# Optimization experiments

Hardware: AMD Instinct MI355X
Metric: run time of the kernel (lower is better)

## Reference

```python
import jax, jax.numpy as jnp
import numpy as np

B, N, M, C = 8, 8192, 2048, 256
EPS = 1e-8


def setup_inputs() -> dict:
    key = jax.random.key(0)
    k1, k2, k3 = jax.random.split(key, 3)
    unknown = jax.random.uniform(k1, (B, N, 3), dtype=jnp.float32)
    known = jax.random.uniform(k2, (B, M, 3), dtype=jnp.float32)
    known_feats = jax.random.normal(k3, (B, C, M), dtype=jnp.float32)
    return {"unknown": unknown, "known": known, "known_feats": known_feats}


def reference(unknown, known, known_feats):
    # three_nn: brute-force squared distances (B, n, m); pointnet2's CUDA
    # three_nn returns SQUARED distances, matching 1/(d2 + eps) weighting.
    diff = unknown[:, :, None, :] - known[:, None, :, :]  # (B, n, m, 3)
    d2 = jnp.sum(diff * diff, axis=-1)                    # (B, n, m)
    neg_d2, idx = jax.lax.top_k(-d2, 3)                   # 3 smallest distances
    dist = -neg_d2                                        # (B, n, 3)
    dist_recip = 1.0 / (dist + EPS)
    weight = dist_recip / jnp.sum(dist_recip, axis=2, keepdims=True)  # (B, n, 3)
    # three_interpolate: gather the 3 neighbor features and weighted-sum.
    feats_t = jnp.swapaxes(known_feats, 1, 2)             # (B, m, C)
    gathered = jax.vmap(lambda f, i: f[i])(feats_t, idx)  # (B, n, 3, C)
    new_features = jnp.einsum("bnkc,bnk->bcn", gathered, weight)  # (B, C, n)
    return new_features
```

## Files before the change

kernel.cpp:

```cpp
#include <hip/hip_runtime.h>


#define BB 8
#define NN 8192
#define MM 2048
#define CC 256
#define EPSV 1e-8f
#define NTH 512
#define NCH 8
#define CHUNK (MM/NCH)
#define PTS 64
#define MARGIN 1e-4f
#define TC 4

#define INS(dd, mi, D0,I0,D1,I1,D2,I2) \
    if ((dd) < D2) { \
        if ((dd) < D1) { D2 = D1; I2 = I1; \
            if ((dd) < D0) { D1 = D0; I1 = I0; D0 = (dd); I0 = (mi); } \
            else           { D1 = (dd); I1 = (mi); } \
        } else { D2 = (dd); I2 = (mi); } }

#define RF(KX,KY,KZ,KQ) \
    __fmaf_rn((KZ), az, __fmaf_rn((KY), ay, __fmaf_rn((KX), ax, (KQ))))

#define S1(KX,KY,KZ,KQ) { \
    const float rr = RF(KX,KY,KZ,KQ); \
    R2 = __builtin_amdgcn_fmed3f(R1, R2, rr); \
    R1 = __builtin_amdgcn_fmed3f(R0, R1, rr); \
    R0 = fminf(R0, rr); }

#define CAP(RR,KX,KY,KZ,MI) \
    if ((RR) <= Tm) { \
        const float dx = ux-(KX), dy = uy-(KY), dz = uz-(KZ); \
        const float d = __fadd_rn(__fadd_rn(__fmul_rn(dx,dx),__fmul_rn(dy,dy)),__fmul_rn(dz,dz)); \
        INS(d, MI, D0,J0,D1,J1,D2,J2) }

typedef unsigned short u16;

__global__ __launch_bounds__(NTH) void nn_scan_kernel(
    const float* __restrict__ unknown,
    const float* __restrict__ known,
    float4* __restrict__ wgt4,
    int4*  __restrict__ idx4)
{
    __shared__ float kxs[MM], kys[MM], kzs[MM], kqs[MM];
    __shared__ float pd[NCH][PTS][3];
    __shared__ u16   si[NCH][PTS][3];
    __shared__ float Tarr[PTS];

    const int tilesPerBatch = NN / PTS;
    const int b    = blockIdx.x / tilesPerBatch;
    const int tile = blockIdx.x % tilesPerBatch;
    const int t    = threadIdx.x;
    const int lane = t & 63;
    const int g    = t >> 6;

    const float* kb = known + (size_t)b * MM * 3;
    for (int idx = t; idx < MM * 3; idx += NTH) {
        const float v  = kb[idx];
        const int   a  = idx % 3;
        const int   mi = idx / 3;
        float* dst = (a == 0) ? kxs : ((a == 1) ? kys : kzs);
        dst[mi] = v;
    }
    __syncthreads();
    for (int m = t; m < MM; m += NTH) {
        const float x = kxs[m], y = kys[m], z = kzs[m];
        kqs[m] = __fmaf_rn(z, z, __fmaf_rn(y, y, x * x));
    }

    const float* u = unknown + ((size_t)b * NN + (size_t)tile * PTS + lane) * 3;
    const float ux = u[0], uy = u[1], uz = u[2];
    const float ax = -2.0f * ux, ay = -2.0f * uy, az = -2.0f * uz;
    __syncthreads();

    float R0 = 1e30f, R1 = 1e30f, R2 = 1e30f;
    const int mbeg = g * CHUNK;
    #pragma unroll 4
    for (int m = mbeg; m < mbeg + CHUNK; m += 4) {
        const float4 x4 = *reinterpret_cast<const float4*>(&kxs[m]);
        const float4 y4 = *reinterpret_cast<const float4*>(&kys[m]);
        const float4 z4 = *reinterpret_cast<const float4*>(&kzs[m]);
        const float4 q4 = *reinterpret_cast<const float4*>(&kqs[m]);
        S1(x4.x, y4.x, z4.x, q4.x)
        S1(x4.y, y4.y, z4.y, q4.y)
        S1(x4.z, y4.z, z4.z, q4.z)
        S1(x4.w, y4.w, z4.w, q4.w)
    }
    pd[g][lane][0] = R0; pd[g][lane][1] = R1; pd[g][lane][2] = R2;
    __syncthreads();

    if (t < PTS) {
        float e0 = 1e30f, e1 = 1e30f, e2 = 1e30f;
        #pragma unroll
        for (int q = 0; q < NCH; ++q) {
            #pragma unroll
            for (int r = 0; r < 3; ++r) {
                const float d = pd[q][t][r];
                e2 = __builtin_amdgcn_fmed3f(e1, e2, d);
                e1 = __builtin_amdgcn_fmed3f(e0, e1, d);
                e0 = fminf(e0, d);
            }
        }
        Tarr[t] = e2 + MARGIN;
    }
    __syncthreads();

    float D0 = 1e30f, D1 = 1e30f, D2 = 1e30f;
    int   J0 = 0,     J1 = 0,     J2 = 0;
    const float Tm = Tarr[lane];

    #pragma unroll 2
    for (int m = mbeg; m < mbeg + CHUNK; m += 4) {
        const float4 x4 = *reinterpret_cast<const float4*>(&kxs[m]);
        const float4 y4 = *reinterpret_cast<const float4*>(&kys[m]);
        const float4 z4 = *reinterpret_cast<const float4*>(&kzs[m]);
        const float4 q4 = *reinterpret_cast<const float4*>(&kqs[m]);
        const float rr0 = RF(x4.x, y4.x, z4.x, q4.x);
        const float rr1 = RF(x4.y, y4.y, z4.y, q4.y);
        const float rr2 = RF(x4.z, y4.z, z4.z, q4.z);
        const float rr3 = RF(x4.w, y4.w, z4.w, q4.w);
        if (fminf(fminf(rr0, rr1), fminf(rr2, rr3)) <= Tm) {
            CAP(rr0, x4.x, y4.x, z4.x, m)
            CAP(rr1, x4.y, y4.y, z4.y, m+1)
            CAP(rr2, x4.z, y4.z, z4.z, m+2)
            CAP(rr3, x4.w, y4.w, z4.w, m+3)
        }
    }

    pd[g][lane][0] = D0; pd[g][lane][1] = D1; pd[g][lane][2] = D2;
    si[g][lane][0] = (u16)J0; si[g][lane][1] = (u16)J1; si[g][lane][2] = (u16)J2;
    __syncthreads();

    if (t < PTS) {
        float e0 = 1e30f, e1 = 1e30f, e2 = 1e30f;
        int   j0 = 0,     j1 = 0,     j2 = 0;
        #pragma unroll
        for (int q = 0; q < NCH; ++q) {
            #pragma unroll
            for (int r = 0; r < 3; ++r) {
                const float d  = pd[q][t][r];
                const int   ii = (int)si[q][t][r];
                INS(d, ii, e0,j0,e1,j1,e2,j2)
            }
        }
        const float r0 = 1.0f / (e0 + EPSV);
        const float r1 = 1.0f / (e1 + EPSV);
        const float r2 = 1.0f / (e2 + EPSV);
        const float rs = r0 + r1 + r2;
        const int gp = b * NN + tile * PTS + t;
        wgt4[gp] = make_float4(r0 / rs, r1 / rs, r2 / rs, 0.0f);
        idx4[gp] = make_int4(j0, j1, j2, 0);
    }
}

__global__ __launch_bounds__(NTH) void interp_kernel(
    const float* __restrict__ feats,
    const float4* __restrict__ wgt4,
    const int4*  __restrict__ idx4,
    float* __restrict__ out)
{
    __shared__ float fbuf[TC * MM];

    const int tilesPerB = CC / TC;
    const int b  = blockIdx.x / tilesPerB;
    const int c0 = (blockIdx.x % tilesPerB) * TC;
    const int t  = threadIdx.x;

    const float4* src = reinterpret_cast<const float4*>(
        feats + ((size_t)b * CC + c0) * MM);
    #pragma unroll
    for (int i = t; i < TC * MM / 4; i += NTH)
        reinterpret_cast<float4*>(fbuf)[i] = src[i];
    __syncthreads();

    #pragma unroll 2
    for (int it = 0; it < NN / NTH; ++it) {
        const int n = it * NTH + t;
        const float4 w = wgt4[b * NN + n];
        const int4   j = idx4[b * NN + n];
        float* ob = out + ((size_t)b * CC + c0) * NN + n;
        #pragma unroll
        for (int cl = 0; cl < TC; ++cl) {
            const float* fr = fbuf + cl * MM;
            ob[(size_t)cl * NN] = w.x * fr[j.x] + w.y * fr[j.y] + w.z * fr[j.z];
        }
    }
}

extern "C" void kernel_launch(void* const* d_in, const int* in_sizes, int n_in,
                              void* d_out, int out_size, void* d_ws, size_t ws_size,
                              hipStream_t stream) {
    const float* unknown = (const float*)d_in[0];
    const float* known   = (const float*)d_in[1];
    const float* feats   = (const float*)d_in[2];
    float* out = (float*)d_out;

    float4* wgt4 = (float4*)d_ws;
    int4*   idx4 = (int4*)((char*)d_ws + (size_t)BB * NN * sizeof(float4));

    nn_scan_kernel<<<BB * (NN / PTS), NTH, 0, stream>>>(unknown, known, wgt4, idx4);
    interp_kernel<<<BB * (CC / TC), NTH, 0, stream>>>(feats, wgt4, idx4, out);
}
```

Measured before the change: 147.4 us.

## Stream packed known points through scalar loads instead of LDS staging

Adds a pre-pass kernel that packs known points into float4 (x,y,z,|k|^2) in the workspace. The scan kernel then drops its LDS staging and reads these wave-uniform values with inline s_load_dwordx16 into scalar registers. The points are broadcast from SGPRs, so the per-point LDS vector loads and the block-wide staging barrier go away. In exchange it adds an extra kernel launch and an s_waitcnt stall on every 8-point group, and depends on the scalar cache serving the loads well.

```diff
diff --git a/kernel.cpp b/kernel.cpp
--- a/kernel.cpp
+++ b/kernel.cpp
@@ -13,6 +13,9 @@
 #define MARGIN 1e-4f
 #define TC 4
 
+typedef unsigned short u16;
+typedef float f16x __attribute__((ext_vector_type(16)));
+
 #define INS(dd, mi, D0,I0,D1,I1,D2,I2) \
     if ((dd) < D2) { \
         if ((dd) < D1) { D2 = D1; I2 = I1; \
@@ -20,30 +23,45 @@
             else           { D1 = (dd); I1 = (mi); } \
         } else { D2 = (dd); I2 = (mi); } }
 
-#define RF(KX,KY,KZ,KQ) \
-    __fmaf_rn((KZ), az, __fmaf_rn((KY), ay, __fmaf_rn((KX), ax, (KQ))))
-
-#define S1(KX,KY,KZ,KQ) { \
-    const float rr = RF(KX,KY,KZ,KQ); \
+#define SLOAD2(A0,A1,PTR) \
+    asm volatile("s_load_dwordx16 %0, %2, 0x0\n\t" \
+                 "s_load_dwordx16 %1, %2, 0x40\n\t" \
+                 "s_waitcnt lgkmcnt(0)" \
+                 : "=s"(A0), "=s"(A1) : "s"(PTR));
+
+#define RFE(A,J) \
+    __fmaf_rn((A)[(J)*4+2], az, __fmaf_rn((A)[(J)*4+1], ay, \
+              __fmaf_rn((A)[(J)*4+0], ax, (A)[(J)*4+3])))
+
+#define S1E(A,J) { \
+    const float rr = RFE(A,J); \
     R2 = __builtin_amdgcn_fmed3f(R1, R2, rr); \
     R1 = __builtin_amdgcn_fmed3f(R0, R1, rr); \
     R0 = fminf(R0, rr); }
 
-#define CAP(RR,KX,KY,KZ,MI) \
+#define CAPX(RR,A,J,MI) \
     if ((RR) <= Tm) { \
-        const float dx = ux-(KX), dy = uy-(KY), dz = uz-(KZ); \
+        const float dx = ux-(A)[(J)*4+0], dy = uy-(A)[(J)*4+1], dz = uz-(A)[(J)*4+2]; \
         const float d = __fadd_rn(__fadd_rn(__fmul_rn(dx,dx),__fmul_rn(dy,dy)),__fmul_rn(dz,dz)); \
         INS(d, MI, D0,J0,D1,J1,D2,J2) }
 
-typedef unsigned short u16;
+__global__ __launch_bounds__(256) void pack_kernel(
+    const float* __restrict__ known, float4* __restrict__ pack)
+{
+    const int i = blockIdx.x * 256 + threadIdx.x;
+    if (i < BB * MM) {
+        const float* k = known + (size_t)i * 3;
+        const float x = k[0], y = k[1], z = k[2];
+        pack[i] = make_float4(x, y, z, __fmaf_rn(z, z, __fmaf_rn(y, y, x * x)));
+    }
+}
 
 __global__ __launch_bounds__(NTH) void nn_scan_kernel(
     const float* __restrict__ unknown,
-    const float* __restrict__ known,
+    const float4* __restrict__ pack,
     float4* __restrict__ wgt4,
     int4*  __restrict__ idx4)
 {
-    __shared__ float kxs[MM], kys[MM], kzs[MM], kqs[MM];
     __shared__ float pd[NCH][PTS][3];
     __shared__ u16   si[NCH][PTS][3];
     __shared__ float Tarr[PTS];
@@ -53,41 +71,27 @@
     const int tile = blockIdx.x % tilesPerBatch;
     const int t    = threadIdx.x;
     const int lane = t & 63;
-    const int g    = t >> 6;
-
-    const float* kb = known + (size_t)b * MM * 3;
-    for (int idx = t; idx < MM * 3; idx += NTH) {
-        const float v  = kb[idx];
-        const int   a  = idx % 3;
-        const int   mi = idx / 3;
-        float* dst = (a == 0) ? kxs : ((a == 1) ? kys : kzs);
-        dst[mi] = v;
-    }
-    __syncthreads();
-    for (int m = t; m < MM; m += NTH) {
-        const float x = kxs[m], y = kys[m], z = kzs[m];
-        kqs[m] = __fmaf_rn(z, z, __fmaf_rn(y, y, x * x));
-    }
+    const int gu   = __builtin_amdgcn_readfirstlane(t >> 6);
 
     const float* u = unknown + ((size_t)b * NN + (size_t)tile * PTS + lane) * 3;
     const float ux = u[0], uy = u[1], uz = u[2];
     const float ax = -2.0f * ux, ay = -2.0f * uy, az = -2.0f * uz;
-    __syncthreads();
+
+    const float4* kp0 = pack + (size_t)b * MM + gu * CHUNK;
+    const int mwave = gu * CHUNK;
 
     float R0 = 1e30f, R1 = 1e30f, R2 = 1e30f;
-    const int mbeg = g * CHUNK;
-    #pragma unroll 4
-    for (int m = mbeg; m < mbeg + CHUNK; m += 4) {
-        const float4 x4 = *reinterpret_cast<const float4*>(&kxs[m]);
-        const float4 y4 = *reinterpret_cast<const float4*>(&kys[m]);
-        const float4 z4 = *reinterpret_cast<const float4*>(&kzs[m]);
-        const float4 q4 = *reinterpret_cast<const float4*>(&kqs[m]);
-        S1(x4.x, y4.x, z4.x, q4.x)
-        S1(x4.y, y4.y, z4.y, q4.y)
-        S1(x4.z, y4.z, z4.z, q4.z)
-        S1(x4.w, y4.w, z4.w, q4.w)
-    }
-    pd[g][lane][0] = R0; pd[g][lane][1] = R1; pd[g][lane][2] = R2;
+    {
+        const float4* kp = kp0;
+        #pragma unroll 2
+        for (int grp = 0; grp < CHUNK / 8; ++grp, kp += 8) {
+            f16x a0, a1;
+            SLOAD2(a0, a1, kp)
+            S1E(a0,0) S1E(a0,1) S1E(a0,2) S1E(a0,3)
+            S1E(a1,0) S1E(a1,1) S1E(a1,2) S1E(a1,3)
+        }
+    }
+    pd[gu][lane][0] = R0; pd[gu][lane][1] = R1; pd[gu][lane][2] = R2;
     __syncthreads();
 
     if (t < PTS) {
@@ -109,27 +113,37 @@
     float D0 = 1e30f, D1 = 1e30f, D2 = 1e30f;
     int   J0 = 0,     J1 = 0,     J2 = 0;
     const float Tm = Tarr[lane];
-
-    #pragma unroll 2
-    for (int m = mbeg; m < mbeg + CHUNK; m += 4) {
-        const float4 x4 = *reinterpret_cast<const float4*>(&kxs[m]);
-        const float4 y4 = *reinterpret_cast<const float4*>(&kys[m]);
-        const float4 z4 = *reinterpret_cast<const float4*>(&kzs[m]);
-        const float4 q4 = *reinterpret_cast<const float4*>(&kqs[m]);
-        const float rr0 = RF(x4.x, y4.x, z4.x, q4.x);
-        const float rr1 = RF(x4.y, y4.y, z4.y, q4.y);
-        const float rr2 = RF(x4.z, y4.z, z4.z, q4.z);
-        const float rr3 = RF(x4.w, y4.w, z4.w, q4.w);
-        if (fminf(fminf(rr0, rr1), fminf(rr2, rr3)) <= Tm) {
-            CAP(rr0, x4.x, y4.x, z4.x, m)
-            CAP(rr1, x4.y, y4.y, z4.y, m+1)
-            CAP(rr2, x4.z, y4.z, z4.z, m+2)
-            CAP(rr3, x4.w, y4.w, z4.w, m+3)
-        }
-    }
-
-    pd[g][lane][0] = D0; pd[g][lane][1] = D1; pd[g][lane][2] = D2;
-    si[g][lane][0] = (u16)J0; si[g][lane][1] = (u16)J1; si[g][lane][2] = (u16)J2;
+    {
+        const float4* kp = kp0;
+        for (int grp = 0; grp < CHUNK / 8; ++grp, kp += 8) {
+            f16x a0, a1;
+            SLOAD2(a0, a1, kp)
+            const int mbase = mwave + grp * 8;
+            {
+                const float rr0 = RFE(a0,0), rr1 = RFE(a0,1);
+                const float rr2 = RFE(a0,2), rr3 = RFE(a0,3);
+                if (fminf(fminf(rr0, rr1), fminf(rr2, rr3)) <= Tm) {
+                    CAPX(rr0, a0,0, mbase+0)
+                    CAPX(rr1, a0,1, mbase+1)
+                    CAPX(rr2, a0,2, mbase+2)
+                    CAPX(rr3, a0,3, mbase+3)
+                }
+            }
+            {
+                const float rr0 = RFE(a1,0), rr1 = RFE(a1,1);
+                const float rr2 = RFE(a1,2), rr3 = RFE(a1,3);
+                if (fminf(fminf(rr0, rr1), fminf(rr2, rr3)) <= Tm) {
+                    CAPX(rr0, a1,0, mbase+4)
+                    CAPX(rr1, a1,1, mbase+5)
+                    CAPX(rr2, a1,2, mbase+6)
+                    CAPX(rr3, a1,3, mbase+7)
+                }
+            }
+        }
+    }
+
+    pd[gu][lane][0] = D0; pd[gu][lane][1] = D1; pd[gu][lane][2] = D2;
+    si[gu][lane][0] = (u16)J0; si[gu][lane][1] = (u16)J1; si[gu][lane][2] = (u16)J2;
     __syncthreads();
 
     if (t < PTS) {
@@ -198,7 +212,9 @@
 
     float4* wgt4 = (float4*)d_ws;
     int4*   idx4 = (int4*)((char*)d_ws + (size_t)BB * NN * sizeof(float4));
-
-    nn_scan_kernel<<<BB * (NN / PTS), NTH, 0, stream>>>(unknown, known, wgt4, idx4);
+    float4* pack = (float4*)((char*)d_ws + 2 * (size_t)BB * NN * 16);
+
+    pack_kernel<<<(BB * MM + 255) / 256, 256, 0, stream>>>(known, pack);
+    nn_scan_kernel<<<BB * (NN / PTS), NTH, 0, stream>>>(unknown, pack, wgt4, idx4);
     interp_kernel<<<BB * (CC / TC), NTH, 0, stream>>>(feats, wgt4, idx4, out);
 }
```

After: 149.8 us. No clear change (+1.6%).
